# Kernel tuning notes

Hardware: AMD Instinct MI355X
Metric: run time of the kernel (lower is better)

The kernel has to match this reference:

```python
import jax, jax.numpy as jnp
import numpy as np

B, S, D = 2, 1024, 2048
L = 4
HQ, HKV, HD = 32, 8, 64
I = 5632
V = 32000
EPS = 1e-5
THETA = 10000.0
SCALE = HD ** -0.5
GROUP = HQ // HKV


def setup_inputs() -> dict:
    key = jax.random.key(0)
    ks = jax.random.split(key, 8)
    s = 0.02
    return {
        "input_ids": jax.random.randint(ks[0], (B, S), 0, V, dtype=jnp.int32),
        "positions": jnp.broadcast_to(jnp.arange(S, dtype=jnp.int32), (B, S)),
        "embed": jax.random.normal(ks[1], (V, D), jnp.float32) * s,
        "w_qkv": jax.random.normal(ks[2], (L, D, (HQ + 2 * HKV) * HD), jnp.float32) * s,
        "w_o": jax.random.normal(ks[3], (L, HQ * HD, D), jnp.float32) * s,
        "w_gate_up": jax.random.normal(ks[4], (L, D, 2 * I), jnp.float32) * s,
        "w_down": jax.random.normal(ks[5], (L, I, D), jnp.float32) * s,
        "ln1_w": jnp.ones((L, D), jnp.float32),
        "ln2_w": jnp.ones((L, D), jnp.float32),
        "norm_w": jnp.ones((D,), jnp.float32),
    }


def rmsnorm(x, w):
    var = jnp.mean(x * x, axis=-1, keepdims=True)
    return x * jax.lax.rsqrt(var + EPS) * w


def rope(positions, x):
    # x: [B, S, H, HD]; neox-style rotate-half RoPE
    inv_freq = 1.0 / (THETA ** (jnp.arange(0, HD, 2, dtype=jnp.float32) / HD))
    ang = positions.astype(jnp.float32)[..., None] * inv_freq  # [B, S, HD/2]
    cos = jnp.cos(ang)[:, :, None, :]
    sin = jnp.sin(ang)[:, :, None, :]
    x1, x2 = jnp.split(x, 2, axis=-1)
    return jnp.concatenate([x1 * cos - x2 * sin, x2 * cos + x1 * sin], axis=-1)


def llama_forward(input_ids, positions, embed, w_qkv, w_o, w_gate_up, w_down,
                  ln1_w, ln2_w, norm_w):
    h = embed[input_ids]                      # [B, S, D]
    res = jnp.zeros_like(h)
    causal = jnp.tril(jnp.ones((S, S), dtype=bool))
    neg = jnp.asarray(jnp.finfo(h.dtype).min, h.dtype)

    def layer(carry, params):
        h, res = carry
        wqkv, wo, wgu, wd, l1, l2 = params
        # fused RMSNorm + residual-add (vllm RMSNorm(x, residual) semantics)
        res = h + res
        h = rmsnorm(res, l1)
        # QKV projection + RoPE
        qkv = h @ wqkv
        q, k, v = jnp.split(qkv, [HQ * HD, (HQ + HKV) * HD], axis=-1)
        q = q.reshape(B, S, HQ, HD)
        k = k.reshape(B, S, HKV, HD)
        v = v.reshape(B, S, HKV, HD)
        q = rope(positions, q)
        k = rope(positions, k)
        # GQA: broadcast kv heads across query groups
        k = jnp.repeat(k, GROUP, axis=2)      # [B, S, HQ, HD]
        v = jnp.repeat(v, GROUP, axis=2)
        scores = jnp.einsum('bqhd,bkhd->bhqk', q, k) * SCALE
        scores = jnp.where(causal, scores, neg)
        attn = jax.nn.softmax(scores, axis=-1)
        o = jnp.einsum('bhqk,bkhd->bqhd', attn, v).reshape(B, S, HQ * HD)
        h = o @ wo
        # post-attention fused RMSNorm + residual
        res = h + res
        h = rmsnorm(res, l2)
        # SwiGLU MLP
        gu = h @ wgu
        g, u = jnp.split(gu, 2, axis=-1)
        h = (jax.nn.silu(g) * u) @ wd
        return (h, res), None

    (h, res), _ = jax.lax.scan(layer, (h, res),
                               (w_qkv, w_o, w_gate_up, w_down, ln1_w, ln2_w))
    return rmsnorm(h + res, norm_w)


def reference(input_ids, positions, embed, w_qkv, w_o, w_gate_up, w_down,
              ln1_w, ln2_w, norm_w):
    return llama_forward(input_ids, positions, embed, w_qkv, w_o, w_gate_up,
                         w_down, ln1_w, ln2_w, norm_w)
```

## Files before the change

kernel.cpp:

```cpp
#include <hip/hip_runtime.h>
#include <hip/hip_bf16.h>

#define B_ 2
#define S_ 1024
#define T_ (B_*S_)
#define D_ 2048
#define L_ 4
#define HQ_ 32
#define HKV_ 8
#define HD_ 64
#define I_ 5632
#define EPS_ 1e-5f
#define SCALE_ 0.125f

typedef __attribute__((ext_vector_type(4))) float  float4v;
typedef __attribute__((ext_vector_type(8))) short  short8v;

#define GLOAD16(g, l) \
  __builtin_amdgcn_global_load_lds((const __attribute__((address_space(1))) void*)(g), \
                                   (__attribute__((address_space(3))) void*)(l), 16, 0, 0)

__device__ __forceinline__ short f2bf(float f) {
  union { float f; unsigned u; } c; c.f = f;
  unsigned u = c.u + 0x7fffu + ((c.u >> 16) & 1u);
  return (short)(u >> 16);
}

__device__ __forceinline__ void xcd_swizzle(int gx, int gy, int& bx, int& by) {
  int nwg = gx * gy;
  int orig = by * gx + bx;
  int q = nwg >> 3, r = nwg & 7;
  int xcd = orig & 7, loc = orig >> 3;
  int swz = (xcd < r ? xcd * (q + 1) : r * (q + 1) + (xcd - r) * q) + loc;
  bx = swz / gy;
  by = swz - bx * gy;
}

__global__ __launch_bounds__(256)
void transpose_bf16(const float* __restrict__ in, short* __restrict__ out,
                    int K, int N) {
  __shared__ float t[64][65];
  const int bx = blockIdx.x * 64;
  const int by = blockIdx.y * 64;
  const int tid = threadIdx.x;
  const int lr = tid >> 4;
  const int lc = (tid & 15) * 4;
  #pragma unroll
  for (int j = 0; j < 64; j += 16) {
    float4v v = *(const float4v*)(in + (size_t)(by + lr + j) * N + bx + lc);
    t[lr + j][lc] = v[0]; t[lr + j][lc + 1] = v[1];
    t[lr + j][lc + 2] = v[2]; t[lr + j][lc + 3] = v[3];
  }
  __syncthreads();
  const int nr = tid >> 3;
  const int kc = (tid & 7) * 8;
  #pragma unroll
  for (int j = 0; j < 64; j += 32) {
    short8v y;
    #pragma unroll
    for (int e = 0; e < 8; e++) y[e] = f2bf(t[kc + e][nr + j]);
    *(short8v*)(out + (size_t)(bx + nr + j) * K + by + kc) = y;
  }
}

__global__ __launch_bounds__(256)
void embed_gather(const int* __restrict__ ids, const float* __restrict__ embed,
                  float* __restrict__ h) {
  size_t i = (size_t)blockIdx.x * 256 + threadIdx.x;
  int t  = (int)(i >> 9);
  int d4 = (int)(i & 511);
  ((float4v*)h)[i] = ((const float4v*)(embed + (size_t)ids[t] * D_))[d4];
}

__global__ __launch_bounds__(256)
void rmsnorm_add(const float* __restrict__ x, float* __restrict__ res,
                 const float* __restrict__ w, void* __restrict__ outp,
                 int first, int bf16out) {
  const int row = blockIdx.x;
  const int tid = threadIdx.x;
  const size_t base = (size_t)row * D_;
  float4v v0 = ((const float4v*)(x + base))[tid * 2];
  float4v v1 = ((const float4v*)(x + base))[tid * 2 + 1];
  if (!first) {
    v0 += ((const float4v*)(res + base))[tid * 2];
    v1 += ((const float4v*)(res + base))[tid * 2 + 1];
  }
  ((float4v*)(res + base))[tid * 2]     = v0;
  ((float4v*)(res + base))[tid * 2 + 1] = v1;
  float ss = v0[0]*v0[0] + v0[1]*v0[1] + v0[2]*v0[2] + v0[3]*v0[3]
           + v1[0]*v1[0] + v1[1]*v1[1] + v1[2]*v1[2] + v1[3]*v1[3];
  #pragma unroll
  for (int off = 32; off > 0; off >>= 1) ss += __shfl_xor(ss, off, 64);
  __shared__ float red[4];
  if ((tid & 63) == 0) red[tid >> 6] = ss;
  __syncthreads();
  float tot = red[0] + red[1] + red[2] + red[3];
  float rs = rsqrtf(tot * (1.0f / D_) + EPS_);
  float4v w0 = ((const float4v*)w)[tid * 2];
  float4v w1 = ((const float4v*)w)[tid * 2 + 1];
  float4v o0 = v0 * rs * w0;
  float4v o1 = v1 * rs * w1;
  if (bf16out) {
    short8v y;
    #pragma unroll
    for (int k = 0; k < 4; k++) { y[k] = f2bf(o0[k]); y[k + 4] = f2bf(o1[k]); }
    ((short8v*)((char*)outp + base * 2))[tid] = y;
  } else {
    float* op = (float*)outp + base;
    ((float4v*)op)[tid * 2]     = o0;
    ((float4v*)op)[tid * 2 + 1] = o1;
  }
}

__global__ __launch_bounds__(512, 4)
void gemm_big128(const short* __restrict__ A, const short* __restrict__ Bt,
                 float* __restrict__ C, int M, int N, int K) {
  __shared__ short sA[2][128 * 64];
  __shared__ short sB[2][128 * 64];
  int bx = blockIdx.x, by = blockIdx.y;
  xcd_swizzle(gridDim.x, gridDim.y, bx, by);
  const int tid  = threadIdx.x;
  const int lane = tid & 63;
  const int wv   = tid >> 6;
  const int wr   = wv >> 2;
  const int wc   = wv & 3;
  const int row0 = by * 128;
  const int col0 = bx * 128;
  const int fr = lane & 15;
  const int g  = lane >> 4;
  const int NT = K >> 6;

  float4v acc[4][2] = {};

  int rS[2], cS[2];
  #pragma unroll
  for (int k = 0; k < 2; k++) {
    int s = tid + k * 512;
    rS[k] = s >> 3;
    cS[k] = (((s & 7) ^ (rS[k] & 7)) << 3);
  }

#define STAGE128(t, buf) do { \
    int k0_ = (t) << 6; \
    _Pragma("unroll") \
    for (int k_ = 0; k_ < 2; k_++) \
      GLOAD16(A  + (size_t)(row0 + rS[k_]) * K + k0_ + cS[k_], \
              &sA[buf][(tid + k_ * 512) * 8]); \
    _Pragma("unroll") \
    for (int k_ = 0; k_ < 2; k_++) \
      GLOAD16(Bt + (size_t)(col0 + rS[k_]) * K + k0_ + cS[k_], \
              &sB[buf][(tid + k_ * 512) * 8]); \
  } while (0)

  STAGE128(0, 0);

  for (int t = 0; t < NT; t++) {
    const int cur = t & 1;
    if (t + 1 < NT) {
      STAGE128(t + 1, cur ^ 1);
      asm volatile("s_waitcnt vmcnt(4)" ::: "memory");
    } else {
      asm volatile("s_waitcnt vmcnt(0)" ::: "memory");
    }
    __builtin_amdgcn_s_barrier();
    __builtin_amdgcn_sched_barrier(0);

    const short* pA = &sA[cur][(wr * 64) * 64];
    const short* pB = &sB[cur][(wc * 32) * 64];
    #pragma unroll
    for (int ks = 0; ks < 2; ks++) {
      const int fswk = ((((ks << 2) | g) ^ (fr & 7)) << 3);
      short8v bfr[2], afr[4];
      #pragma unroll
      for (int ni = 0; ni < 2; ni++)
        bfr[ni] = *(const short8v*)(pB + (ni * 16 + fr) * 64 + fswk);
      #pragma unroll
      for (int m4 = 0; m4 < 4; m4++)
        afr[m4] = *(const short8v*)(pA + (m4 * 16 + fr) * 64 + fswk);
      __builtin_amdgcn_s_setprio(1);
      #pragma unroll
      for (int m4 = 0; m4 < 4; m4++)
        #pragma unroll
        for (int ni = 0; ni < 2; ni++)
          acc[m4][ni] = __builtin_amdgcn_mfma_f32_16x16x32_bf16(
              afr[m4], bfr[ni], acc[m4][ni], 0, 0, 0);
      __builtin_amdgcn_s_setprio(0);
    }
    asm volatile("" ::: "memory");
    __builtin_amdgcn_s_barrier();
  }

  #pragma unroll
  for (int m4 = 0; m4 < 4; m4++)
    #pragma unroll
    for (int ni = 0; ni < 2; ni++) {
      size_t base = (size_t)(row0 + wr * 64 + m4 * 16 + g * 4) * N
                    + col0 + wc * 32 + ni * 16 + fr;
      #pragma unroll
      for (int r = 0; r < 4; r++)
        C[base + (size_t)r * N] = acc[m4][ni][r];
    }
#undef STAGE128
}

__global__ __launch_bounds__(512, 2)
void gemm_glu_big(const short* __restrict__ A, const short* __restrict__ Bt,
                  short* __restrict__ mlp, int K) {
  __shared__ short sA[2][128 * 64];
  __shared__ short sG[2][128 * 64];
  __shared__ short sU[2][128 * 64];
  int bx = blockIdx.x, by = blockIdx.y;
  xcd_swizzle(gridDim.x, gridDim.y, bx, by);
  const int tid  = threadIdx.x;
  const int lane = tid & 63;
  const int wv   = tid >> 6;
  const int wr   = wv >> 2;
  const int wc   = wv & 3;
  const int row0 = by * 128;
  const int col0 = bx * 128;
  const int fr = lane & 15;
  const int g  = lane >> 4;
  const int NT = K >> 6;

  float4v accg[4][2] = {};
  float4v accu[4][2] = {};

  int rS[2], cS[2];
  #pragma unroll
  for (int k = 0; k < 2; k++) {
    int s = tid + k * 512;
    rS[k] = s >> 3;
    cS[k] = (((s & 7) ^ (rS[k] & 7)) << 3);
  }

#define STAGEGLU(t, buf) do { \
    int k0_ = (t) << 6; \
    _Pragma("unroll") \
    for (int k_ = 0; k_ < 2; k_++) \
      GLOAD16(A  + (size_t)(row0 + rS[k_]) * K + k0_ + cS[k_], \
              &sA[buf][(tid + k_ * 512) * 8]); \
    _Pragma("unroll") \
    for (int k_ = 0; k_ < 2; k_++) \
      GLOAD16(Bt + (size_t)(col0 + rS[k_]) * K + k0_ + cS[k_], \
              &sG[buf][(tid + k_ * 512) * 8]); \
    _Pragma("unroll") \
    for (int k_ = 0; k_ < 2; k_++) \
      GLOAD16(Bt + (size_t)(col0 + I_ + rS[k_]) * K + k0_ + cS[k_], \
              &sU[buf][(tid + k_ * 512) * 8]); \
  } while (0)

  STAGEGLU(0, 0);

  for (int t = 0; t < NT; t++) {
    const int cur = t & 1;
    if (t + 1 < NT) {
      STAGEGLU(t + 1, cur ^ 1);
      asm volatile("s_waitcnt vmcnt(6)" ::: "memory");
    } else {
      asm volatile("s_waitcnt vmcnt(0)" ::: "memory");
    }
    __builtin_amdgcn_s_barrier();
    __builtin_amdgcn_sched_barrier(0);

    const short* pA = &sA[cur][(wr * 64) * 64];
    const short* pG = &sG[cur][(wc * 32) * 64];
    const short* pU = &sU[cur][(wc * 32) * 64];
    #pragma unroll
    for (int ks = 0; ks < 2; ks++) {
      const int fswk = ((((ks << 2) | g) ^ (fr & 7)) << 3);
      short8v bg[2], bu[2], afr[4];
      #pragma unroll
      for (int ni = 0; ni < 2; ni++) {
        bg[ni] = *(const short8v*)(pG + (ni * 16 + fr) * 64 + fswk);
        bu[ni] = *(const short8v*)(pU + (ni * 16 + fr) * 64 + fswk);
      }
      #pragma unroll
      for (int m4 = 0; m4 < 4; m4++)
        afr[m4] = *(const short8v*)(pA + (m4 * 16 + fr) * 64 + fswk);
      __builtin_amdgcn_s_setprio(1);
      #pragma unroll
      for (int m4 = 0; m4 < 4; m4++)
        #pragma unroll
        for (int ni = 0; ni < 2; ni++) {
          accg[m4][ni] = __builtin_amdgcn_mfma_f32_16x16x32_bf16(
              afr[m4], bg[ni], accg[m4][ni], 0, 0, 0);
          accu[m4][ni] = __builtin_amdgcn_mfma_f32_16x16x32_bf16(
              afr[m4], bu[ni], accu[m4][ni], 0, 0, 0);
        }
      __builtin_amdgcn_s_setprio(0);
    }
    asm volatile("" ::: "memory");
    __builtin_amdgcn_s_barrier();
  }

  #pragma unroll
  for (int m4 = 0; m4 < 4; m4++)
    #pragma unroll
    for (int ni = 0; ni < 2; ni++) {
      size_t base = (size_t)(row0 + wr * 64 + m4 * 16 + g * 4) * I_
                    + col0 + wc * 32 + ni * 16 + fr;
      #pragma unroll
      for (int r = 0; r < 4; r++) {
        float gv = accg[m4][ni][r], uv = accu[m4][ni][r];
        mlp[base + (size_t)r * I_] = f2bf(gv / (1.0f + __expf(-gv)) * uv);
      }
    }
#undef STAGEGLU
}

__global__ __launch_bounds__(512, 4)
void gemm_qkv_big(const short* __restrict__ A, const short* __restrict__ Bt,
                  const float* __restrict__ tab, short* __restrict__ qbf,
                  short* __restrict__ kbf, short* __restrict__ vbf, int K) {
  __shared__ short sA[2][128 * 64];
  __shared__ short sB[2][128 * 64];
  int bx = blockIdx.x, by = blockIdx.y;
  xcd_swizzle(gridDim.x, gridDim.y, bx, by);
  const int tid  = threadIdx.x;
  const int lane = tid & 63;
  const int wv   = tid >> 6;
  const int wm   = (wv >> 1) * 32;
  const int wn   = (wv & 1) * 64;
  const int row0 = by * 128;
  const int col0 = bx * 128;
  const int fr = lane & 15;
  const int g  = lane >> 4;
  const int NT = K >> 6;

  float4v acc[2][4] = {};

  int rS[2], cS[2];
  #pragma unroll
  for (int k = 0; k < 2; k++) {
    int s = tid + k * 512;
    rS[k] = s >> 3;
    cS[k] = (((s & 7) ^ (rS[k] & 7)) << 3);
  }

#define STAGEQKV(t, buf) do { \
    int k0_ = (t) << 6; \
    _Pragma("unroll") \
    for (int k_ = 0; k_ < 2; k_++) \
      GLOAD16(A  + (size_t)(row0 + rS[k_]) * K + k0_ + cS[k_], \
              &sA[buf][(tid + k_ * 512) * 8]); \
    _Pragma("unroll") \
    for (int k_ = 0; k_ < 2; k_++) \
      GLOAD16(Bt + (size_t)(col0 + rS[k_]) * K + k0_ + cS[k_], \
              &sB[buf][(tid + k_ * 512) * 8]); \
  } while (0)

  STAGEQKV(0, 0);

  for (int t = 0; t < NT; t++) {
    const int cur = t & 1;
    if (t + 1 < NT) {
      STAGEQKV(t + 1, cur ^ 1);
      asm volatile("s_waitcnt vmcnt(4)" ::: "memory");
    } else {
      asm volatile("s_waitcnt vmcnt(0)" ::: "memory");
    }
    __builtin_amdgcn_s_barrier();
    __builtin_amdgcn_sched_barrier(0);

    const short* pA = &sA[cur][wm * 64];
    const short* pB = &sB[cur][wn * 64];
    #pragma unroll
    for (int ks = 0; ks < 2; ks++) {
      const int fswk = ((((ks << 2) | g) ^ (fr & 7)) << 3);
      short8v afr[2], bfr[4];
      #pragma unroll
      for (int m2 = 0; m2 < 2; m2++)
        afr[m2] = *(const short8v*)(pA + (m2 * 16 + fr) * 64 + fswk);
      #pragma unroll
      for (int ni = 0; ni < 4; ni++)
        bfr[ni] = *(const short8v*)(pB + (ni * 16 + fr) * 64 + fswk);
      __builtin_amdgcn_s_setprio(1);
      #pragma unroll
      for (int m2 = 0; m2 < 2; m2++)
        #pragma unroll
        for (int ni = 0; ni < 4; ni++)
          acc[m2][ni] = __builtin_amdgcn_mfma_f32_16x16x32_bf16(
              afr[m2], bfr[ni], acc[m2][ni], 0, 0, 0);
      __builtin_amdgcn_s_setprio(0);
    }
    asm volatile("" ::: "memory");
    __builtin_amdgcn_s_barrier();
  }

  const int head = (col0 + wn) >> 6;
  if (head < HQ_ + HKV_) {
    const float sc = (head < HQ_) ? SCALE_ : 1.0f;
    short* dst = (head < HQ_) ? qbf : kbf;
    const int hh = (head < HQ_) ? head : head - HQ_;
    const int HN = (head < HQ_) ? HQ_ : HKV_;
    #pragma unroll
    for (int m2 = 0; m2 < 2; m2++)
      #pragma unroll
      for (int jj = 0; jj < 2; jj++)
        #pragma unroll
        for (int r = 0; r < 4; r++) {
          int m = row0 + wm + m2 * 16 + g * 4 + r;
          int b = m >> 10, s = m & (S_ - 1);
          int d1 = jj * 16 + fr;
          float x1 = acc[m2][jj][r], x2 = acc[m2][jj + 2][r];
          const float* tb = tab + (size_t)m * 64 + d1 * 2;
          float c = tb[0], sn = tb[1];
          size_t base = ((size_t)((b * HN + hh) * S_ + s)) * HD_;
          dst[base + d1]      = f2bf((x1 * c - x2 * sn) * sc);
          dst[base + d1 + 32] = f2bf((x2 * c + x1 * sn) * sc);
        }
  } else {
    const int vh = head - HQ_ - HKV_;
    #pragma unroll
    for (int m2 = 0; m2 < 2; m2++)
      #pragma unroll
      for (int ni = 0; ni < 4; ni++)
        #pragma unroll
        for (int r = 0; r < 4; r++) {
          int m = row0 + wm + m2 * 16 + g * 4 + r;
          int b = m >> 10, s = m & (S_ - 1);
          vbf[((size_t)((b * HKV_ + vh) * S_ + s)) * HD_ + ni * 16 + fr] =
              f2bf(acc[m2][ni][r]);
        }
  }
#undef STAGEQKV
}

__global__ __launch_bounds__(256)
void rope_table(const int* __restrict__ pos, float* __restrict__ tab) {
  int i = blockIdx.x * 256 + threadIdx.x;
  int t = i >> 5, ii = i & 31;
  float p = (float)pos[t];
  float freq = __expf(-(float)ii * (9.210340371976184f / 32.0f));
  float ang = p * freq;
  tab[2 * i]     = cosf(ang);
  tab[2 * i + 1] = sinf(ang);
}

#define KPAD 68

__global__ __launch_bounds__(256)
void transpose_v(const short* __restrict__ vbf, short* __restrict__ vtbf) {
  __shared__ short sv[64 * KPAD];
  const int jt = blockIdx.x, kh = blockIdx.y, b = blockIdx.z;
  const int tid = threadIdx.x;
  const short* src = vbf + ((size_t)((b * HKV_ + kh) * S_ + jt * 64)) * HD_;
  #pragma unroll
  for (int it = 0; it < 2; it++) {
    int c = it * 256 + tid;
    int rr = c >> 3, ch = (c & 7) * 8;
    *(short8v*)(&sv[rr * KPAD + ch]) = *(const short8v*)(src + (size_t)rr * HD_ + ch);
  }
  __syncthreads();
  const int dc = tid >> 2;
  const int jc = (tid & 3) * 16;
  short8v o1, o2;
  #pragma unroll
  for (int k = 0; k < 8; k++) o1[k] = sv[(jc + k) * KPAD + dc];
  #pragma unroll
  for (int k = 0; k < 8; k++) o2[k] = sv[(jc + 8 + k) * KPAD + dc];
  short* od = vtbf + ((size_t)((b * HKV_ + kh) * HD_ + dc)) * S_ + jt * 64 + jc;
  *(short8v*)od       = o1;
  *(short8v*)(od + 8) = o2;
}

__global__ __launch_bounds__(256)
void attn_mfma(const short* __restrict__ qbf, const short* __restrict__ kbf,
               const short* __restrict__ vtbf, short* __restrict__ obf) {
  __shared__ short sK[64 * KPAD];
  __shared__ short sVt[64 * KPAD];
  __shared__ short sP[4][16 * KPAD];
  const int qb = blockIdx.x;
  const int h  = blockIdx.y;
  const int b  = blockIdx.z;
  const int kh = h >> 2;
  const int tid  = threadIdx.x;
  const int lane = tid & 63;
  const int wv   = tid >> 6;
  const int q0 = qb * 64;
  const int cc = lane & 15;
  const int g  = lane >> 4;

  short8v qf0, qf1;
  {
    const short* qrow = qbf + ((size_t)((b * HQ_ + h) * S_ + q0 + wv * 16 + cc)) * HD_;
    qf0 = *(const short8v*)(qrow + g * 8);
    qf1 = *(const short8v*)(qrow + g * 8 + 32);
  }
  float4v accO[4] = {};
  float m_r[4], l_r[4];
  #pragma unroll
  for (int r = 0; r < 4; r++) { m_r[r] = -1e30f; l_r[r] = 0.f; }

  const short* kb = kbf  + ((size_t)(b * HKV_ + kh)) * S_ * HD_;
  const short* vb = vtbf + ((size_t)(b * HKV_ + kh)) * HD_ * S_;

  const int rr0 = tid >> 3;
  const int ch0 = (tid & 7) * 8;
  const int rr1 = 32 + rr0;

  short8v kr0 = *(const short8v*)(kb + (size_t)rr0 * HD_ + ch0);
  short8v kr1 = *(const short8v*)(kb + (size_t)rr1 * HD_ + ch0);
  short8v vr0 = *(const short8v*)(vb + (size_t)rr0 * S_ + ch0);
  short8v vr1 = *(const short8v*)(vb + (size_t)rr1 * S_ + ch0);

  for (int jt = 0; jt <= qb; jt++) {
    const int j0 = jt * 64;
    __syncthreads();
    *(short8v*)(&sK[rr0 * KPAD + ch0])  = kr0;
    *(short8v*)(&sK[rr1 * KPAD + ch0])  = kr1;
    *(short8v*)(&sVt[rr0 * KPAD + ch0]) = vr0;
    *(short8v*)(&sVt[rr1 * KPAD + ch0]) = vr1;
    __syncthreads();

    if (jt < qb) {
      const int j0n = j0 + 64;
      kr0 = *(const short8v*)(kb + (size_t)(j0n + rr0) * HD_ + ch0);
      kr1 = *(const short8v*)(kb + (size_t)(j0n + rr1) * HD_ + ch0);
      vr0 = *(const short8v*)(vb + (size_t)rr0 * S_ + j0n + ch0);
      vr1 = *(const short8v*)(vb + (size_t)rr1 * S_ + j0n + ch0);
    }

    float4v sc[4] = {};
    #pragma unroll
    for (int ct = 0; ct < 4; ct++) {
      short8v k0 = *(const short8v*)(&sK[(ct * 16 + cc) * KPAD + g * 8]);
      short8v k1 = *(const short8v*)(&sK[(ct * 16 + cc) * KPAD + g * 8 + 32]);
      __builtin_amdgcn_s_setprio(1);
      sc[ct] = __builtin_amdgcn_mfma_f32_16x16x32_bf16(qf0, k0, sc[ct], 0, 0, 0);
      sc[ct] = __builtin_amdgcn_mfma_f32_16x16x32_bf16(qf1, k1, sc[ct], 0, 0, 0);
      __builtin_amdgcn_s_setprio(0);
    }
    if (jt == qb) {
      #pragma unroll
      for (int ct = 0; ct < 4; ct++)
        #pragma unroll
        for (int r = 0; r < 4; r++)
          if (j0 + ct * 16 + cc > q0 + wv * 16 + g * 4 + r) sc[ct][r] = -1e30f;
    }
    float corr[4];
    #pragma unroll
    for (int r = 0; r < 4; r++) {
      float pm = fmaxf(fmaxf(sc[0][r], sc[1][r]), fmaxf(sc[2][r], sc[3][r]));
      pm = fmaxf(pm, __shfl_xor(pm, 1, 64));
      pm = fmaxf(pm, __shfl_xor(pm, 2, 64));
      pm = fmaxf(pm, __shfl_xor(pm, 4, 64));
      pm = fmaxf(pm, __shfl_xor(pm, 8, 64));
      float mn = fmaxf(m_r[r], pm);
      corr[r] = __expf(m_r[r] - mn);
      m_r[r] = mn;
      float rs = 0.f;
      #pragma unroll
      for (int ct = 0; ct < 4; ct++) {
        float p = __expf(sc[ct][r] - mn);
        sc[ct][r] = p;
        rs += p;
      }
      rs += __shfl_xor(rs, 1, 64);
      rs += __shfl_xor(rs, 2, 64);
      rs += __shfl_xor(rs, 4, 64);
      rs += __shfl_xor(rs, 8, 64);
      l_r[r] = l_r[r] * corr[r] + rs;
    }
    #pragma unroll
    for (int ct = 0; ct < 4; ct++)
      #pragma unroll
      for (int r = 0; r < 4; r++)
        sP[wv][(g * 4 + r) * KPAD + ct * 16 + cc] = f2bf(sc[ct][r]);
    #pragma unroll
    for (int dt = 0; dt < 4; dt++)
      #pragma unroll
      for (int r = 0; r < 4; r++)
        accO[dt][r] *= corr[r];
    short8v pf0 = *(const short8v*)(&sP[wv][cc * KPAD + g * 8]);
    short8v pf1 = *(const short8v*)(&sP[wv][cc * KPAD + g * 8 + 32]);
    #pragma unroll
    for (int dt = 0; dt < 4; dt++) {
      short8v v0 = *(const short8v*)(&sVt[(dt * 16 + cc) * KPAD + g * 8]);
      short8v v1 = *(const short8v*)(&sVt[(dt * 16 + cc) * KPAD + g * 8 + 32]);
      __builtin_amdgcn_s_setprio(1);
      accO[dt] = __builtin_amdgcn_mfma_f32_16x16x32_bf16(pf0, v0, accO[dt], 0, 0, 0);
      accO[dt] = __builtin_amdgcn_mfma_f32_16x16x32_bf16(pf1, v1, accO[dt], 0, 0, 0);
      __builtin_amdgcn_s_setprio(0);
    }
  }
  #pragma unroll
  for (int dt = 0; dt < 4; dt++)
    #pragma unroll
    for (int r = 0; r < 4; r++) {
      int q = q0 + wv * 16 + g * 4 + r;
      obf[((size_t)(b * S_ + q)) * 2048 + h * 64 + dt * 16 + cc] = f2bf(accO[dt][r] / l_r[r]);
    }
}

extern "C" void kernel_launch(void* const* d_in, const int* in_sizes, int n_in,
                              void* d_out, int out_size, void* d_ws, size_t ws_size,
                              hipStream_t stream) {
  const int*   ids   = (const int*)d_in[0];
  const int*   pos   = (const int*)d_in[1];
  const float* embed = (const float*)d_in[2];
  const float* w_qkv = (const float*)d_in[3];
  const float* w_o   = (const float*)d_in[4];
  const float* w_gu  = (const float*)d_in[5];
  const float* w_dn  = (const float*)d_in[6];
  const float* ln1   = (const float*)d_in[7];
  const float* ln2   = (const float*)d_in[8];
  const float* normw = (const float*)d_in[9];
  float* out = (float*)d_out;

  char* p = (char*)d_ws;
  short* wT    = (short*)p; p += (size_t)11264 * 2048 * 2;
  float* h     = (float*)p; p += (size_t)T_ * D_ * 4;
  float* res   = (float*)p; p += (size_t)T_ * D_ * 4;
  short* hnbf  = (short*)p; p += (size_t)T_ * D_ * 2;
  short* obf   = (short*)p; p += (size_t)T_ * D_ * 2;
  short* mlpbf = (short*)p; p += (size_t)T_ * I_ * 2;
  float* tab   = (float*)p; p += (size_t)T_ * 64 * 4;
  short* qbf   = (short*)p; p += (size_t)B_ * HQ_ * S_ * HD_ * 2;
  short* kbf   = (short*)p; p += (size_t)B_ * HKV_ * S_ * HD_ * 2;
  short* vbf   = (short*)p; p += (size_t)B_ * HKV_ * S_ * HD_ * 2;
  short* vtbf  = (short*)p; p += (size_t)B_ * HKV_ * HD_ * S_ * 2;

  embed_gather<<<T_ * D_ / 4 / 256, 256, 0, stream>>>(ids, embed, h);
  rope_table<<<T_ * 32 / 256, 256, 0, stream>>>(pos, tab);

  for (int l = 0; l < L_; l++) {
    rmsnorm_add<<<T_, 256, 0, stream>>>(h, res, ln1 + l * D_, hnbf, l == 0 ? 1 : 0, 1);

    transpose_bf16<<<dim3(3072 / 64, 2048 / 64), 256, 0, stream>>>(
        w_qkv + (size_t)l * 2048 * 3072, wT, 2048, 3072);
    gemm_qkv_big<<<dim3(3072 / 128, T_ / 128), 512, 0, stream>>>(
        hnbf, wT, tab, qbf, kbf, vbf, 2048);

    transpose_v<<<dim3(16, 8, 2), 256, 0, stream>>>(vbf, vtbf);
    attn_mfma<<<dim3(16, 32, 2), 256, 0, stream>>>(qbf, kbf, vtbf, obf);

    transpose_bf16<<<dim3(2048 / 64, 2048 / 64), 256, 0, stream>>>(
        w_o + (size_t)l * 2048 * 2048, wT, 2048, 2048);
    gemm_big128<<<dim3(2048 / 128, T_ / 128), 512, 0, stream>>>(
        obf, wT, h, T_, 2048, 2048);

    rmsnorm_add<<<T_, 256, 0, stream>>>(h, res, ln2 + l * D_, hnbf, 0, 1);

    transpose_bf16<<<dim3(11264 / 64, 2048 / 64), 256, 0, stream>>>(
        w_gu + (size_t)l * 2048 * 11264, wT, 2048, 11264);
    gemm_glu_big<<<dim3(I_ / 128, T_ / 128), 512, 0, stream>>>(
        hnbf, wT, mlpbf, 2048);

    transpose_bf16<<<dim3(2048 / 64, 5632 / 64), 256, 0, stream>>>(
        w_dn + (size_t)l * 5632 * 2048, wT, 5632, 2048);
    gemm_big128<<<dim3(2048 / 128, T_ / 128), 512, 0, stream>>>(
        mlpbf, wT, h, T_, 2048, 5632);
  }
  rmsnorm_add<<<T_, 256, 0, stream>>>(h, res, normw, out, 0, 0);
}
```

Measured before the change: 1.740 ms.

## Fuse residual add into GEMM epilogues and lazily rescale attention softmax

Output and down projection GEMMs now accumulate directly into the residual buffer, so the rmsnorm kernel only reads the residual instead of reading two buffers and writing one back. The attention loop skips the running-max update and accumulator rescale unless a row's max grows by more than a threshold. This cuts memory traffic in the norm and some ALU work in attention, at the cost of read-modify-write epilogues and a stale max bounded by e^8.

```diff
diff --git a/kernel.cpp b/kernel.cpp
--- a/kernel.cpp
+++ b/kernel.cpp
@@ -73,20 +73,22 @@
 }
 
 __global__ __launch_bounds__(256)
-void rmsnorm_add(const float* __restrict__ x, float* __restrict__ res,
-                 const float* __restrict__ w, void* __restrict__ outp,
-                 int first, int bf16out) {
+void rmsnorm_kernel(const float* __restrict__ x, float* __restrict__ res,
+                    const float* __restrict__ w, void* __restrict__ outp,
+                    int first, int bf16out) {
   const int row = blockIdx.x;
   const int tid = threadIdx.x;
   const size_t base = (size_t)row * D_;
-  float4v v0 = ((const float4v*)(x + base))[tid * 2];
-  float4v v1 = ((const float4v*)(x + base))[tid * 2 + 1];
-  if (!first) {
-    v0 += ((const float4v*)(res + base))[tid * 2];
-    v1 += ((const float4v*)(res + base))[tid * 2 + 1];
-  }
-  ((float4v*)(res + base))[tid * 2]     = v0;
-  ((float4v*)(res + base))[tid * 2 + 1] = v1;
+  float4v v0, v1;
+  if (first) {
+    v0 = ((const float4v*)(x + base))[tid * 2];
+    v1 = ((const float4v*)(x + base))[tid * 2 + 1];
+    ((float4v*)(res + base))[tid * 2]     = v0;
+    ((float4v*)(res + base))[tid * 2 + 1] = v1;
+  } else {
+    v0 = ((const float4v*)(res + base))[tid * 2];
+    v1 = ((const float4v*)(res + base))[tid * 2 + 1];
+  }
   float ss = v0[0]*v0[0] + v0[1]*v0[1] + v0[2]*v0[2] + v0[3]*v0[3]
            + v1[0]*v1[0] + v1[1]*v1[1] + v1[2]*v1[2] + v1[3]*v1[3];
   #pragma unroll
@@ -114,7 +116,7 @@
 
 __global__ __launch_bounds__(512, 4)
 void gemm_big128(const short* __restrict__ A, const short* __restrict__ Bt,
-                 float* __restrict__ C, int M, int N, int K) {
+                 float* __restrict__ C, int M, int N, int K, int addto) {
   __shared__ short sA[2][128 * 64];
   __shared__ short sB[2][128 * 64];
   int bx = blockIdx.x, by = blockIdx.y;
@@ -196,9 +198,15 @@
     for (int ni = 0; ni < 2; ni++) {
       size_t base = (size_t)(row0 + wr * 64 + m4 * 16 + g * 4) * N
                     + col0 + wc * 32 + ni * 16 + fr;
-      #pragma unroll
-      for (int r = 0; r < 4; r++)
-        C[base + (size_t)r * N] = acc[m4][ni][r];
+      if (addto) {
+        #pragma unroll
+        for (int r = 0; r < 4; r++)
+          C[base + (size_t)r * N] += acc[m4][ni][r];
+      } else {
+        #pragma unroll
+        for (int r = 0; r < 4; r++)
+          C[base + (size_t)r * N] = acc[m4][ni][r];
+      }
     }
 #undef STAGE128
 }
@@ -538,7 +546,7 @@
         for (int r = 0; r < 4; r++)
           if (j0 + ct * 16 + cc > q0 + wv * 16 + g * 4 + r) sc[ct][r] = -1e30f;
     }
-    float corr[4];
+    float pmv[4], dmax = -1e30f;
     #pragma unroll
     for (int r = 0; r < 4; r++) {
       float pm = fmaxf(fmaxf(sc[0][r], sc[1][r]), fmaxf(sc[2][r], sc[3][r]));
@@ -546,13 +554,30 @@
       pm = fmaxf(pm, __shfl_xor(pm, 2, 64));
       pm = fmaxf(pm, __shfl_xor(pm, 4, 64));
       pm = fmaxf(pm, __shfl_xor(pm, 8, 64));
-      float mn = fmaxf(m_r[r], pm);
-      corr[r] = __expf(m_r[r] - mn);
-      m_r[r] = mn;
+      pmv[r] = pm;
+      dmax = fmaxf(dmax, pm - m_r[r]);
+    }
+    if (!__all(dmax <= 8.0f)) {
+      float corr[4];
+      #pragma unroll
+      for (int r = 0; r < 4; r++) {
+        float mn = fmaxf(m_r[r], pmv[r]);
+        corr[r] = __expf(m_r[r] - mn);
+        m_r[r] = mn;
+        l_r[r] *= corr[r];
+      }
+      #pragma unroll
+      for (int dt = 0; dt < 4; dt++)
+        #pragma unroll
+        for (int r = 0; r < 4; r++)
+          accO[dt][r] *= corr[r];
+    }
+    #pragma unroll
+    for (int r = 0; r < 4; r++) {
       float rs = 0.f;
       #pragma unroll
       for (int ct = 0; ct < 4; ct++) {
-        float p = __expf(sc[ct][r] - mn);
+        float p = __expf(sc[ct][r] - m_r[r]);
         sc[ct][r] = p;
         rs += p;
       }
@@ -560,18 +585,13 @@
       rs += __shfl_xor(rs, 2, 64);
       rs += __shfl_xor(rs, 4, 64);
       rs += __shfl_xor(rs, 8, 64);
-      l_r[r] = l_r[r] * corr[r] + rs;
+      l_r[r] += rs;
     }
     #pragma unroll
     for (int ct = 0; ct < 4; ct++)
       #pragma unroll
       for (int r = 0; r < 4; r++)
         sP[wv][(g * 4 + r) * KPAD + ct * 16 + cc] = f2bf(sc[ct][r]);
-    #pragma unroll
-    for (int dt = 0; dt < 4; dt++)
-      #pragma unroll
-      for (int r = 0; r < 4; r++)
-        accO[dt][r] *= corr[r];
     short8v pf0 = *(const short8v*)(&sP[wv][cc * KPAD + g * 8]);
     short8v pf1 = *(const short8v*)(&sP[wv][cc * KPAD + g * 8 + 32]);
     #pragma unroll
@@ -625,7 +645,8 @@
   rope_table<<<T_ * 32 / 256, 256, 0, stream>>>(pos, tab);
 
   for (int l = 0; l < L_; l++) {
-    rmsnorm_add<<<T_, 256, 0, stream>>>(h, res, ln1 + l * D_, hnbf, l == 0 ? 1 : 0, 1);
+    rmsnorm_kernel<<<T_, 256, 0, stream>>>(h, res, ln1 + l * D_, hnbf,
+                                           l == 0 ? 1 : 0, 1);
 
     transpose_bf16<<<dim3(3072 / 64, 2048 / 64), 256, 0, stream>>>(
         w_qkv + (size_t)l * 2048 * 3072, wT, 2048, 3072);
@@ -638,9 +659,9 @@
     transpose_bf16<<<dim3(2048 / 64, 2048 / 64), 256, 0, stream>>>(
         w_o + (size_t)l * 2048 * 2048, wT, 2048, 2048);
     gemm_big128<<<dim3(2048 / 128, T_ / 128), 512, 0, stream>>>(
-        obf, wT, h, T_, 2048, 2048);
-
-    rmsnorm_add<<<T_, 256, 0, stream>>>(h, res, ln2 + l * D_, hnbf, 0, 1);
+        obf, wT, res, T_, 2048, 2048, 1);
+
+    rmsnorm_kernel<<<T_, 256, 0, stream>>>(nullptr, res, ln2 + l * D_, hnbf, 0, 1);
 
     transpose_bf16<<<dim3(11264 / 64, 2048 / 64), 256, 0, stream>>>(
         w_gu + (size_t)l * 2048 * 11264, wT, 2048, 11264);
@@ -650,7 +671,7 @@
     transpose_bf16<<<dim3(2048 / 64, 5632 / 64), 256, 0, stream>>>(
         w_dn + (size_t)l * 5632 * 2048, wT, 5632, 2048);
     gemm_big128<<<dim3(2048 / 128, T_ / 128), 512, 0, stream>>>(
-        mlpbf, wT, h, T_, 2048, 5632);
-  }
-  rmsnorm_add<<<T_, 256, 0, stream>>>(h, res, normw, out, 0, 0);
-}
+        mlpbf, wT, res, T_, 2048, 5632, 1);
+  }
+  rmsnorm_kernel<<<T_, 256, 0, stream>>>(nullptr, res, normw, out, 0, 0);
+}
```

After: 1.739 ms. About the same (-0.1%).
